# Kernel tuning notes

Measured on AMD Instinct MI355X. Metric: run time of the kernel, lower is better.

## Reference

```python
import jax, jax.numpy as jnp
import numpy as np

TAU = 100.0
DT = 20.0
ALPHA = DT / TAU  # 0.2, leaky-integration coefficient


def setup_inputs() -> dict:
    key = jax.random.key(0)
    k1, k2, k3, k4, k5 = jax.random.split(key, 5)
    S, B, I, H = 512, 128, 512, 1024
    # scale params like torch Linear default init (uniform +-1/sqrt(fan_in))
    x = jax.random.normal(k1, (S, B, I), dtype=jnp.float32)
    W_in = jax.random.uniform(k2, (H, I), jnp.float32, -1.0, 1.0) / np.sqrt(I)
    b_in = jax.random.uniform(k3, (H,), jnp.float32, -1.0, 1.0) / np.sqrt(I)
    W_hh = jax.random.uniform(k4, (H, H), jnp.float32, -1.0, 1.0) / np.sqrt(H)
    b_hh = jax.random.uniform(k5, (H,), jnp.float32, -1.0, 1.0) / np.sqrt(H)
    return {"x": x, "W_in": W_in, "b_in": b_in, "W_hh": W_hh, "b_hh": b_hh}


def reference(x, W_in, b_in, W_hh, b_hh):
    # x: (S, B, I). Precompute input projection once (torch code recomputes it,
    # but the math is identical): (S, B, H)
    input_projection = jnp.einsum('sbi,hi->sbh', x, W_in) + b_in

    def step(h, xt):
        # xt: (B, H) precomputed input2h(input[t])
        h_new = jax.nn.relu(xt + h @ W_hh.T + b_hh)
        h = h * (1.0 - ALPHA) + h_new * ALPHA
        return h, h

    B, H = x.shape[1], W_in.shape[0]
    h0 = jnp.zeros((B, H), dtype=x.dtype)
    hidden, output = jax.lax.scan(step, h0, input_projection)
    return output, hidden, input_projection
```

## Files before the change

kernel.cpp:

```cpp
#include <hip/hip_runtime.h>
#include <hip/hip_bf16.h>


typedef __attribute__((ext_vector_type(8))) short short8;
typedef __attribute__((ext_vector_type(4))) float f32x4;
typedef __attribute__((ext_vector_type(4))) uint  uint4v;

#define S_LEN 512
#define BATCH 128
#define IN_DIM 512
#define HID 1024

__device__ __forceinline__ ushort f2bf(float f) {
    __hip_bfloat16 h = __float2bfloat16(f);
    return *reinterpret_cast<ushort*>(&h);
}

__global__ __launch_bounds__(256) void ip_gemm(const float* __restrict__ x,
                                               const float* __restrict__ W_in,
                                               const float* __restrict__ b_in,
                                               float* __restrict__ ip) {
    __shared__ __align__(16) ushort As[128 * 32];
    __shared__ __align__(16) ushort Bs[64 * 32];
    const int tid  = threadIdx.x;
    const int lane = tid & 63;
    const int w    = tid >> 6;
    const int mt   = blockIdx.x >> 4;
    const int nt   = blockIdx.x & 15;
    const long Mbase = (long)mt * 128;
    const int  Nbase = nt * 64;

    const int sr = tid >> 2;
    const int sk = (tid & 3) * 8;

    f32x4 a00={0,0,0,0}, a01={0,0,0,0}, a02={0,0,0,0}, a03={0,0,0,0};
    f32x4 a10={0,0,0,0}, a11={0,0,0,0}, a12={0,0,0,0}, a13={0,0,0,0};

    const int ar0   = w * 32 + (lane & 15);
    const int ar1   = ar0 + 16;
    const int kb    = ((lane >> 4) * 8) * 2;
    const int aoff0 = (ar0 * 64 + kb) ^ ((ar0 & 7) << 4);
    const int aoff1 = (ar1 * 64 + kb) ^ ((ar1 & 7) << 4);
    const int boff  = ((lane & 15) * 64 + kb) ^ (((lane & 15) & 7) << 4);
    const int soff0 = (sr * 64 + sk * 2) ^ ((sr & 7) << 4);
    const int soff1 = ((sr + 64) * 64 + sk * 2) ^ ((sr & 7) << 4);

    for (int kc = 0; kc < IN_DIM; kc += 32) {
        const float* ap0 = x + (Mbase + sr) * IN_DIM + kc + sk;
        const float* ap1 = ap0 + (size_t)64 * IN_DIM;
        const float* wp  = W_in + (size_t)(Nbase + sr) * IN_DIM + kc + sk;
        f32x4 x0l = ((const f32x4*)ap0)[0], x0h = ((const f32x4*)ap0)[1];
        f32x4 x1l = ((const f32x4*)ap1)[0], x1h = ((const f32x4*)ap1)[1];
        f32x4 bl  = ((const f32x4*)wp)[0],  bh  = ((const f32x4*)wp)[1];
        short8 av0, av1, bv;
#pragma unroll
        for (int j = 0; j < 4; ++j) {
            av0[j]     = (short)f2bf(x0l[j]);
            av0[4 + j] = (short)f2bf(x0h[j]);
            av1[j]     = (short)f2bf(x1l[j]);
            av1[4 + j] = (short)f2bf(x1h[j]);
            bv[j]      = (short)f2bf(bl[j]);
            bv[4 + j]  = (short)f2bf(bh[j]);
        }
        __syncthreads();
        *(short8*)((char*)As + soff0) = av0;
        *(short8*)((char*)As + soff1) = av1;
        *(short8*)((char*)Bs + soff0) = bv;
        __syncthreads();

        short8 A0 = *(const short8*)((char*)As + aoff0);
        short8 A1 = *(const short8*)((char*)As + aoff1);
        short8 B0 = *(const short8*)((char*)Bs + boff);
        short8 B1 = *(const short8*)((char*)Bs + boff + 1024);
        short8 B2 = *(const short8*)((char*)Bs + boff + 2048);
        short8 B3 = *(const short8*)((char*)Bs + boff + 3072);
        a00 = __builtin_amdgcn_mfma_f32_16x16x32_bf16(A0, B0, a00, 0, 0, 0);
        a01 = __builtin_amdgcn_mfma_f32_16x16x32_bf16(A0, B1, a01, 0, 0, 0);
        a02 = __builtin_amdgcn_mfma_f32_16x16x32_bf16(A0, B2, a02, 0, 0, 0);
        a03 = __builtin_amdgcn_mfma_f32_16x16x32_bf16(A0, B3, a03, 0, 0, 0);
        a10 = __builtin_amdgcn_mfma_f32_16x16x32_bf16(A1, B0, a10, 0, 0, 0);
        a11 = __builtin_amdgcn_mfma_f32_16x16x32_bf16(A1, B1, a11, 0, 0, 0);
        a12 = __builtin_amdgcn_mfma_f32_16x16x32_bf16(A1, B2, a12, 0, 0, 0);
        a13 = __builtin_amdgcn_mfma_f32_16x16x32_bf16(A1, B3, a13, 0, 0, 0);
    }

    const int nl   = lane & 15;
    const int mrow = w * 32 + (lane >> 4) * 4;
    const float bi0 = b_in[Nbase + nl];
    const float bi1 = b_in[Nbase + 16 + nl];
    const float bi2 = b_in[Nbase + 32 + nl];
    const float bi3 = b_in[Nbase + 48 + nl];
#pragma unroll
    for (int j = 0; j < 4; ++j) {
        float* op0 = ip + (Mbase + mrow + j) * HID + Nbase + nl;
        op0[0]  = a00[j] + bi0;
        op0[16] = a01[j] + bi1;
        op0[32] = a02[j] + bi2;
        op0[48] = a03[j] + bi3;
        float* op1 = op0 + (size_t)16 * HID;
        op1[0]  = a10[j] + bi0;
        op1[16] = a11[j] + bi1;
        op1[32] = a12[j] + bi2;
        op1[48] = a13[j] + bi3;
    }
}

__global__ __launch_bounds__(256, 1) void ctrnn_rec(const float* __restrict__ whh,
                                                    const float* __restrict__ b_hh,
                                                    const float* __restrict__ ip,
                                                    float* __restrict__ out,
                                                    float* __restrict__ hidden,
                                                    ushort* __restrict__ hbuf) {
    const int tid  = threadIdx.x;
    const int lane = tid & 63;
    const int w    = tid >> 6;
    const int bi   = blockIdx.x & 7;
    const int ni   = blockIdx.x >> 3;

    __shared__ __align__(16) float P[2][4][16][68];

    const int arow = lane & 15;
    const int kgrp = (lane >> 4) * 8;

    short8 wf[4][8];
#pragma unroll
    for (int g = 0; g < 4; ++g)
#pragma unroll
        for (int kk = 0; kk < 8; ++kk) {
            const float* wp = whh + (size_t)(ni * 64 + g * 16 + arow) * HID
                              + w * 256 + kk * 32 + kgrp;
            f32x4 w0 = *(const f32x4*)wp;
            f32x4 w1 = *(const f32x4*)(wp + 4);
            short8 f;
#pragma unroll
            for (int j = 0; j < 4; ++j) {
                f[j]     = (short)f2bf(w0[j]);
                f[4 + j] = (short)f2bf(w1[j]);
            }
            wf[g][kk] = f;
        }

    const int eb = tid >> 4;
    const int n0 = (tid & 15) * 4;
    const f32x4 bias4 = *(const f32x4*)&b_hh[ni * 64 + n0];
    const float* xbase = ip + (size_t)(bi * 16 + eb) * HID + ni * 64 + n0;
    f32x4 hprev = {0, 0, 0, 0};
    f32x4 xtv     = *(const f32x4*)xbase;
    f32x4 xt_next = xtv;

    for (int t = 0; t < S_LEN; ++t) {
        f32x4 acc = {0, 0, 0, 0};
        if (t > 0) {
            const uint sexp = (((t - 1) >> 1) & 1) ? 0x80008000u : 0u;
            const ushort* hs = hbuf + (size_t)((t - 1) & 1) * BATCH * HID
                               + (size_t)(bi * 16 + arow) * HID + w * 256 + kgrp;
            uint4v h0, h1, h2, h3, h4, h5, h6, h7;
            long spin = 0;
            for (;;) {
#define LDA(reg, kk)                                                            \
                asm volatile("global_load_dwordx4 %0, %1, off sc0 sc1"          \
                             : "=v"(reg) : "v"(hs + (kk) * 32) : "memory")
                LDA(h0, 0); LDA(h1, 1); LDA(h2, 2); LDA(h3, 3);
                LDA(h4, 4); LDA(h5, 5); LDA(h6, 6); LDA(h7, 7);
#undef LDA
                asm volatile("s_waitcnt vmcnt(0)" ::: "memory");
                __builtin_amdgcn_sched_barrier(0);
                uint4v o = (h0 ^ sexp) | (h1 ^ sexp) | (h2 ^ sexp) | (h3 ^ sexp)
                         | (h4 ^ sexp) | (h5 ^ sexp) | (h6 ^ sexp) | (h7 ^ sexp);
                uint bad = (o[0] | o[1] | o[2] | o[3]) & 0x80008000u;
                if (__all(bad == 0)) break;
                if (++spin > (1L << 20)) break;
            }
            h0 &= 0x7FFF7FFFu; h1 &= 0x7FFF7FFFu; h2 &= 0x7FFF7FFFu; h3 &= 0x7FFF7FFFu;
            h4 &= 0x7FFF7FFFu; h5 &= 0x7FFF7FFFu; h6 &= 0x7FFF7FFFu; h7 &= 0x7FFF7FFFu;
            __builtin_amdgcn_sched_barrier(0);

            if (t + 1 < S_LEN)
                xt_next = *(const f32x4*)(xbase + (size_t)(t + 1) * BATCH * HID);

            f32x4 a0 = {0,0,0,0}, a1 = {0,0,0,0}, a2 = {0,0,0,0}, a3 = {0,0,0,0};
#define STEP(hk, kk)                                                                 \
            a0 = __builtin_amdgcn_mfma_f32_16x16x32_bf16(*(short8*)&hk, wf[0][kk], a0, 0, 0, 0); \
            a1 = __builtin_amdgcn_mfma_f32_16x16x32_bf16(*(short8*)&hk, wf[1][kk], a1, 0, 0, 0); \
            a2 = __builtin_amdgcn_mfma_f32_16x16x32_bf16(*(short8*)&hk, wf[2][kk], a2, 0, 0, 0); \
            a3 = __builtin_amdgcn_mfma_f32_16x16x32_bf16(*(short8*)&hk, wf[3][kk], a3, 0, 0, 0)
            STEP(h0, 0); STEP(h1, 1); STEP(h2, 2); STEP(h3, 3);
            STEP(h4, 4); STEP(h5, 5); STEP(h6, 6); STEP(h7, 7);
#undef STEP

            const int cur = t & 1;
#pragma unroll
            for (int j = 0; j < 4; ++j) {
                const int br = (lane >> 4) * 4 + j;
                P[cur][w][br][arow]      = a0[j];
                P[cur][w][br][16 + arow] = a1[j];
                P[cur][w][br][32 + arow] = a2[j];
                P[cur][w][br][48 + arow] = a3[j];
            }
            __syncthreads();

            f32x4 r0 = *(const f32x4*)&P[cur][0][eb][n0];
            f32x4 r1 = *(const f32x4*)&P[cur][1][eb][n0];
            f32x4 r2 = *(const f32x4*)&P[cur][2][eb][n0];
            f32x4 r3 = *(const f32x4*)&P[cur][3][eb][n0];
            acc = (r0 + r1) + (r2 + r3);
        } else {
            xt_next = *(const f32x4*)(xbase + (size_t)1 * BATCH * HID);
        }

        f32x4 hw;
#pragma unroll
        for (int j = 0; j < 4; ++j) {
            float hn = xtv[j] + acc[j] + bias4[j];
            hn       = hn > 0.0f ? hn : 0.0f;
            hw[j]    = hprev[j] * 0.8f + 0.2f * hn;
        }
        hprev = hw;

        const uint sbit = ((t >> 1) & 1) ? 0x80008000u : 0u;
        uint2 pk;
        pk.x = ((uint)f2bf(hw[0]) | ((uint)f2bf(hw[1]) << 16)) | sbit;
        pk.y = ((uint)f2bf(hw[2]) | ((uint)f2bf(hw[3]) << 16)) | sbit;
        ushort* hdst = hbuf + (size_t)(t & 1) * BATCH * HID
                       + (size_t)(bi * 16 + eb) * HID + ni * 64 + n0;
        asm volatile("global_store_dwordx2 %0, %1, off sc0 sc1" :: "v"(hdst), "v"(pk) : "memory");

        float* od = out + (size_t)t * BATCH * HID + (size_t)(bi * 16 + eb) * HID + ni * 64 + n0;
        *(f32x4*)od = hw;
        if (t == S_LEN - 1) {
            float* hd = hidden + (size_t)(bi * 16 + eb) * HID + ni * 64 + n0;
            *(f32x4*)hd = hw;
        }
        xtv = xt_next;
    }
}

extern "C" void kernel_launch(void* const* d_in, const int* in_sizes, int n_in,
                              void* d_out, int out_size, void* d_ws, size_t ws_size,
                              hipStream_t stream) {
    const float* x    = (const float*)d_in[0];
    const float* W_in = (const float*)d_in[1];
    const float* b_in = (const float*)d_in[2];
    const float* W_hh = (const float*)d_in[3];
    const float* b_hh = (const float*)d_in[4];

    float* out    = (float*)d_out;
    float* hidden = out + (size_t)S_LEN * BATCH * HID;
    float* ip     = hidden + (size_t)BATCH * HID;

    char* ws = (char*)d_ws;
    ushort* hbuf = (ushort*)ws;

    hipMemsetAsync(hbuf, 0xFF, (size_t)2 * BATCH * HID * sizeof(ushort), stream);
    ip_gemm<<<(65536 / 128) * (HID / 64), 256, 0, stream>>>(x, W_in, b_in, ip);
    ctrnn_rec<<<128, 256, 0, stream>>>(W_hh, b_hh, ip, out, hidden, hbuf);
}
```

Baseline: 1.675 ms.

## Widen input-projection GEMM tile to 128x128 and move xt prefetch after the reduction

```diff
diff --git a/kernel.cpp b/kernel.cpp
--- a/kernel.cpp
+++ b/kernel.cpp
@@ -21,88 +21,79 @@
                                                const float* __restrict__ b_in,
                                                float* __restrict__ ip) {
     __shared__ __align__(16) ushort As[128 * 32];
-    __shared__ __align__(16) ushort Bs[64 * 32];
+    __shared__ __align__(16) ushort Bs[128 * 32];
     const int tid  = threadIdx.x;
     const int lane = tid & 63;
     const int w    = tid >> 6;
-    const int mt   = blockIdx.x >> 4;
-    const int nt   = blockIdx.x & 15;
+    const int mt   = blockIdx.x >> 3;
+    const int nt   = blockIdx.x & 7;
     const long Mbase = (long)mt * 128;
-    const int  Nbase = nt * 64;
+    const int  Nbase = nt * 128;
 
     const int sr = tid >> 2;
     const int sk = (tid & 3) * 8;
 
-    f32x4 a00={0,0,0,0}, a01={0,0,0,0}, a02={0,0,0,0}, a03={0,0,0,0};
-    f32x4 a10={0,0,0,0}, a11={0,0,0,0}, a12={0,0,0,0}, a13={0,0,0,0};
+    f32x4 c00={0,0,0,0},c01={0,0,0,0},c02={0,0,0,0},c03={0,0,0,0};
+    f32x4 c04={0,0,0,0},c05={0,0,0,0},c06={0,0,0,0},c07={0,0,0,0};
+    f32x4 c10={0,0,0,0},c11={0,0,0,0},c12={0,0,0,0},c13={0,0,0,0};
+    f32x4 c14={0,0,0,0},c15={0,0,0,0},c16={0,0,0,0},c17={0,0,0,0};
 
     const int ar0   = w * 32 + (lane & 15);
     const int ar1   = ar0 + 16;
-    const int kb    = ((lane >> 4) * 8) * 2;
+    const int kb    = (lane >> 4) * 16;
     const int aoff0 = (ar0 * 64 + kb) ^ ((ar0 & 7) << 4);
     const int aoff1 = (ar1 * 64 + kb) ^ ((ar1 & 7) << 4);
     const int boff  = ((lane & 15) * 64 + kb) ^ (((lane & 15) & 7) << 4);
     const int soff0 = (sr * 64 + sk * 2) ^ ((sr & 7) << 4);
-    const int soff1 = ((sr + 64) * 64 + sk * 2) ^ ((sr & 7) << 4);
+    const int soff1 = soff0 + 4096;
 
     for (int kc = 0; kc < IN_DIM; kc += 32) {
         const float* ap0 = x + (Mbase + sr) * IN_DIM + kc + sk;
         const float* ap1 = ap0 + (size_t)64 * IN_DIM;
-        const float* wp  = W_in + (size_t)(Nbase + sr) * IN_DIM + kc + sk;
+        const float* wp0 = W_in + (size_t)(Nbase + sr) * IN_DIM + kc + sk;
+        const float* wp1 = wp0 + (size_t)64 * IN_DIM;
         f32x4 x0l = ((const f32x4*)ap0)[0], x0h = ((const f32x4*)ap0)[1];
         f32x4 x1l = ((const f32x4*)ap1)[0], x1h = ((const f32x4*)ap1)[1];
-        f32x4 bl  = ((const f32x4*)wp)[0],  bh  = ((const f32x4*)wp)[1];
-        short8 av0, av1, bv;
+        f32x4 b0l = ((const f32x4*)wp0)[0], b0h = ((const f32x4*)wp0)[1];
+        f32x4 b1l = ((const f32x4*)wp1)[0], b1h = ((const f32x4*)wp1)[1];
+        short8 av0, av1, bv0, bv1;
 #pragma unroll
         for (int j = 0; j < 4; ++j) {
-            av0[j]     = (short)f2bf(x0l[j]);
-            av0[4 + j] = (short)f2bf(x0h[j]);
-            av1[j]     = (short)f2bf(x1l[j]);
-            av1[4 + j] = (short)f2bf(x1h[j]);
-            bv[j]      = (short)f2bf(bl[j]);
-            bv[4 + j]  = (short)f2bf(bh[j]);
+            av0[j] = (short)f2bf(x0l[j]); av0[4+j] = (short)f2bf(x0h[j]);
+            av1[j] = (short)f2bf(x1l[j]); av1[4+j] = (short)f2bf(x1h[j]);
+            bv0[j] = (short)f2bf(b0l[j]); bv0[4+j] = (short)f2bf(b0h[j]);
+            bv1[j] = (short)f2bf(b1l[j]); bv1[4+j] = (short)f2bf(b1h[j]);
         }
         __syncthreads();
         *(short8*)((char*)As + soff0) = av0;
         *(short8*)((char*)As + soff1) = av1;
-        *(short8*)((char*)Bs + soff0) = bv;
+        *(short8*)((char*)Bs + soff0) = bv0;
+        *(short8*)((char*)Bs + soff1) = bv1;
         __syncthreads();
 
         short8 A0 = *(const short8*)((char*)As + aoff0);
         short8 A1 = *(const short8*)((char*)As + aoff1);
-        short8 B0 = *(const short8*)((char*)Bs + boff);
-        short8 B1 = *(const short8*)((char*)Bs + boff + 1024);
-        short8 B2 = *(const short8*)((char*)Bs + boff + 2048);
-        short8 B3 = *(const short8*)((char*)Bs + boff + 3072);
-        a00 = __builtin_amdgcn_mfma_f32_16x16x32_bf16(A0, B0, a00, 0, 0, 0);
-        a01 = __builtin_amdgcn_mfma_f32_16x16x32_bf16(A0, B1, a01, 0, 0, 0);
-        a02 = __builtin_amdgcn_mfma_f32_16x16x32_bf16(A0, B2, a02, 0, 0, 0);
-        a03 = __builtin_amdgcn_mfma_f32_16x16x32_bf16(A0, B3, a03, 0, 0, 0);
-        a10 = __builtin_amdgcn_mfma_f32_16x16x32_bf16(A1, B0, a10, 0, 0, 0);
-        a11 = __builtin_amdgcn_mfma_f32_16x16x32_bf16(A1, B1, a11, 0, 0, 0);
-        a12 = __builtin_amdgcn_mfma_f32_16x16x32_bf16(A1, B2, a12, 0, 0, 0);
-        a13 = __builtin_amdgcn_mfma_f32_16x16x32_bf16(A1, B3, a13, 0, 0, 0);
+#define BSTEP(g)                                                                     \
+        { short8 Bv = *(const short8*)((char*)Bs + boff + 1024 * (g));               \
+          c0##g = __builtin_amdgcn_mfma_f32_16x16x32_bf16(A0, Bv, c0##g, 0, 0, 0);   \
+          c1##g = __builtin_amdgcn_mfma_f32_16x16x32_bf16(A1, Bv, c1##g, 0, 0, 0); }
+        BSTEP(0); BSTEP(1); BSTEP(2); BSTEP(3);
+        BSTEP(4); BSTEP(5); BSTEP(6); BSTEP(7);
+#undef BSTEP
     }
 
     const int nl   = lane & 15;
     const int mrow = w * 32 + (lane >> 4) * 4;
-    const float bi0 = b_in[Nbase + nl];
-    const float bi1 = b_in[Nbase + 16 + nl];
-    const float bi2 = b_in[Nbase + 32 + nl];
-    const float bi3 = b_in[Nbase + 48 + nl];
-#pragma unroll
-    for (int j = 0; j < 4; ++j) {
-        float* op0 = ip + (Mbase + mrow + j) * HID + Nbase + nl;
-        op0[0]  = a00[j] + bi0;
-        op0[16] = a01[j] + bi1;
-        op0[32] = a02[j] + bi2;
-        op0[48] = a03[j] + bi3;
-        float* op1 = op0 + (size_t)16 * HID;
-        op1[0]  = a10[j] + bi0;
-        op1[16] = a11[j] + bi1;
-        op1[32] = a12[j] + bi2;
-        op1[48] = a13[j] + bi3;
-    }
+#define EPI(g)                                                                        \
+    { const float bi_ = b_in[Nbase + (g) * 16 + nl];                                  \
+      _Pragma("unroll")                                                               \
+      for (int j = 0; j < 4; ++j) {                                                   \
+          float* op0 = ip + (Mbase + mrow + j) * HID + Nbase + (g) * 16 + nl;         \
+          op0[0] = c0##g[j] + bi_;                                                    \
+          op0[(size_t)16 * HID] = c1##g[j] + bi_;                                     \
+      } }
+    EPI(0); EPI(1); EPI(2); EPI(3); EPI(4); EPI(5); EPI(6); EPI(7);
+#undef EPI
 }
 
 __global__ __launch_bounds__(256, 1) void ctrnn_rec(const float* __restrict__ whh,
@@ -175,9 +166,6 @@
             h4 &= 0x7FFF7FFFu; h5 &= 0x7FFF7FFFu; h6 &= 0x7FFF7FFFu; h7 &= 0x7FFF7FFFu;
             __builtin_amdgcn_sched_barrier(0);
 
-            if (t + 1 < S_LEN)
-                xt_next = *(const f32x4*)(xbase + (size_t)(t + 1) * BATCH * HID);
-
             f32x4 a0 = {0,0,0,0}, a1 = {0,0,0,0}, a2 = {0,0,0,0}, a3 = {0,0,0,0};
 #define STEP(hk, kk)                                                                 \
             a0 = __builtin_amdgcn_mfma_f32_16x16x32_bf16(*(short8*)&hk, wf[0][kk], a0, 0, 0, 0); \
@@ -204,9 +192,10 @@
             f32x4 r2 = *(const f32x4*)&P[cur][2][eb][n0];
             f32x4 r3 = *(const f32x4*)&P[cur][3][eb][n0];
             acc = (r0 + r1) + (r2 + r3);
-        } else {
-            xt_next = *(const f32x4*)(xbase + (size_t)1 * BATCH * HID);
-        }
+        }
+
+        if (t + 1 < S_LEN)
+            xt_next = *(const f32x4*)(xbase + (size_t)(t + 1) * BATCH * HID);
 
         f32x4 hw;
 #pragma unroll
@@ -252,6 +241,6 @@
     ushort* hbuf = (ushort*)ws;
 
     hipMemsetAsync(hbuf, 0xFF, (size_t)2 * BATCH * HID * sizeof(ushort), stream);
-    ip_gemm<<<(65536 / 128) * (HID / 64), 256, 0, stream>>>(x, W_in, b_in, ip);
+    ip_gemm<<<(65536 / 128) * (HID / 128), 256, 0, stream>>>(x, W_in, b_in, ip);
     ctrnn_rec<<<128, 256, 0, stream>>>(W_hh, b_hh, ip, out, hidden, hbuf);
 }
```

Result: faster. 1.377 ms, median of 2 (-17.8%).
